# Kernel optimization log

Hardware: AMD Instinct MI355X
Metric: run time of the kernel (lower is better)

The kernel has to match this reference:

```python
import jax, jax.numpy as jnp
import numpy as np

B, T, D, H, P = 2, 2048, 1024, 16, 64  # batch, seq, d_model, heads, head_dim


def setup_inputs() -> dict:
    key = jax.random.key(0)
    ks = jax.random.split(key, 8)
    s = 0.02
    return {
        "Q": jax.random.normal(ks[0], (B, T, D), jnp.float32),
        "K": jax.random.normal(ks[1], (B, T, D), jnp.float32),
        "V": jax.random.normal(ks[2], (B, T, D), jnp.float32),
        "mask": jnp.ones((B, 1, 1, T), jnp.float32),
        "WQ": jax.random.normal(ks[3], (H, D, P), jnp.float32) * s,
        "WK": jax.random.normal(ks[4], (H, D, P), jnp.float32) * s,
        "WV": jax.random.normal(ks[5], (H, D, P), jnp.float32) * s,
        "rel_emb": jax.random.normal(ks[6], (2 * T - 1, P), jnp.float32) * s,
        "dense_W": jax.random.normal(ks[7], (H * P, D), jnp.float32) * s,
        "dense_b": jnp.zeros((D,), jnp.float32),
    }


def reference(Q, K, V, mask, WQ, WK, WV, rel_emb, dense_W, dense_b):
    # multi-head projections: (B,T,D) x (H,D,P) -> (B,H,T,P)
    q = jnp.einsum("btd,hdp->bhtp", Q, WQ)
    k = jnp.einsum("btd,hdp->bhtp", K, WK)
    v = jnp.einsum("btd,hdp->bhtp", V, WV)

    Tq = q.shape[2]
    # Shaw-style additive relative positional encoding from Q:
    # bias[b,h,i,j] = q[b,h,i] . rel_emb[j - i + T - 1]
    a = jnp.einsum("bhtp,rp->bhtr", q, rel_emb)          # (B,H,T,2T-1)
    rel_idx = jnp.arange(Tq)[None, :] - jnp.arange(Tq)[:, None] + (Tq - 1)  # (T,T)
    rpe = jnp.take_along_axis(a, rel_idx[None, None], axis=-1)              # (B,H,T,T)

    scale = 1.0 / jnp.sqrt(jnp.asarray(P, q.dtype))
    energies = (jnp.einsum("bhtp,bhsp->bhts", q, k) + rpe) * scale
    energies = energies + (1.0 - mask) * -1e9
    alphas = jax.nn.softmax(energies, axis=-1)
    ctx = jnp.einsum("bhts,bhsp->bhtp", alphas, v)        # (B,H,T,P)

    ctx = jnp.transpose(ctx, (0, 2, 1, 3)).reshape(ctx.shape[0], Tq, H * P)
    return ctx @ dense_W + dense_b
```

## Files before the change

### kernel.cpp

```cpp
#include <hip/hip_runtime.h>
#include <hip/hip_bf16.h>

typedef __bf16 bf16_t;
typedef __bf16 bf16x2 __attribute__((ext_vector_type(2)));
typedef __bf16 bf16x8 __attribute__((ext_vector_type(8)));
typedef float f32x4 __attribute__((ext_vector_type(4)));

#define QSCALE 0.1803368801111396f
#define MLOG2E 1.4426950408889634f
#define MCONST 12.0f

__device__ __forceinline__ f32x4 mfma16(bf16x8 a, bf16x8 b, f32x4 c) {
  return __builtin_amdgcn_mfma_f32_16x16x32_bf16(a, b, c, 0, 0, 0);
}

#define GLDS16(gsrc, ldst)                                                     \
  __builtin_amdgcn_global_load_lds(                                            \
      (const __attribute__((address_space(1))) void*)(gsrc),                   \
      (__attribute__((address_space(3))) void*)(ldst), 16, 0, 0)

__device__ __forceinline__ unsigned pack2(float a, float b) {
  bf16x2 t = {(bf16_t)a, (bf16_t)b};
  return __builtin_bit_cast(unsigned, t);
}
__device__ __forceinline__ unsigned short bbits(bf16_t v) {
  return __builtin_bit_cast(unsigned short, v);
}

__global__ void conv_kernel(const float* __restrict__ Q,
                            const float* __restrict__ K,
                            const float* __restrict__ V,
                            const float* __restrict__ WQ,
                            const float* __restrict__ WK,
                            const float* __restrict__ WV,
                            const float* __restrict__ dW,
                            bf16_t* __restrict__ qf, bf16_t* __restrict__ kf,
                            bf16_t* __restrict__ vf, bf16_t* __restrict__ wqf,
                            bf16_t* __restrict__ wkf, bf16_t* __restrict__ wvf,
                            bf16_t* __restrict__ dwf) {
  const int y = blockIdx.y;
  const float* s;
  bf16_t* d;
  size_t n;
  switch (y) {
    case 0: s = Q;  d = qf;  n = 4194304; break;
    case 1: s = K;  d = kf;  n = 4194304; break;
    case 2: s = V;  d = vf;  n = 4194304; break;
    case 3: s = WQ; d = wqf; n = 1048576; break;
    case 4: s = WK; d = wkf; n = 1048576; break;
    case 5: s = WV; d = wvf; n = 1048576; break;
    default: s = dW; d = dwf; n = 1048576; break;
  }
  size_t i = ((size_t)blockIdx.x * 256 + threadIdx.x) * 8;
  if (i >= n) return;
  float4 a = *(const float4*)(s + i);
  float4 b = *(const float4*)(s + i + 4);
  uint4 u = {pack2(a.x, a.y), pack2(a.z, a.w), pack2(b.x, b.y),
             pack2(b.z, b.w)};
  *(uint4*)(d + i) = u;
}

__global__ void prep_kernel(const float* __restrict__ rel,
                            const float* __restrict__ mask,
                            bf16_t* __restrict__ relb,
                            float* __restrict__ mbias) {
  int idx = blockIdx.x * 256 + threadIdx.x;
  if (idx < 4096 * 64) {
    int row = idx >> 6;
    int col = idx & 63;
    int sr = row > 4094 ? 4094 : row;
    relb[idx] = (bf16_t)rel[sr * 64 + col];
  } else {
    int j = idx - 4096 * 64;
    if (j < 4096) mbias[j] = (1.0f - mask[j]) * -1e9f * MLOG2E;
  }
}

__global__ __launch_bounds__(256) void proj_gemm_kernel(
    const bf16_t* __restrict__ Qf, const bf16_t* __restrict__ Kf,
    const bf16_t* __restrict__ Vf, const bf16_t* __restrict__ WQf,
    const bf16_t* __restrict__ WKf, const bf16_t* __restrict__ WVf,
    bf16_t* __restrict__ qb, bf16_t* __restrict__ kb,
    bf16_t* __restrict__ vb) {
  const int z = blockIdx.z;
  const bf16_t* A = z == 0 ? Qf : (z == 1 ? Kf : Vf);
  const bf16_t* W = z == 0 ? WQf : (z == 1 ? WKf : WVf);
  bf16_t* out = z == 0 ? qb : (z == 1 ? kb : vb);
  const float scale = z == 0 ? QSCALE : 1.0f;

  __shared__ bf16_t As[128][72];
  __shared__ bf16_t Bs[128][72];
  const int tid = threadIdx.x;
  const int lane = tid & 63;
  const int wid = tid >> 6;
  const int wm = wid >> 1, wn = wid & 1;
  const int row0 = blockIdx.x * 128;
  const int col0 = blockIdx.y * 128;
  const int lr = lane & 15;
  const int lk = (lane >> 4) * 8;

  f32x4 acc[4][4];
#pragma unroll
  for (int m = 0; m < 4; m++)
#pragma unroll
    for (int n = 0; n < 4; n++) acc[m][n] = {0.f, 0.f, 0.f, 0.f};

  for (int kt = 0; kt < 1024; kt += 64) {
#pragma unroll
    for (int i = 0; i < 4; i++) {
      int c = tid + i * 256;
      int row = c >> 3;
      int k8 = (c & 7) * 8;
      *(uint4*)&As[row][k8] =
          *(const uint4*)(A + (size_t)(row0 + row) * 1024 + kt + k8);
    }
#pragma unroll
    for (int i = 0; i < 4; i++) {
      int c = tid + i * 256;
      int col = c & 127;
      int k8 = (c >> 7) * 8;
      int gcol = col0 + col;
      int h = gcol >> 6, p = gcol & 63;
      const bf16_t* src = W + (size_t)h * 65536 + (size_t)(kt + k8) * 64 + p;
      unsigned short b0 = bbits(src[0]), b1 = bbits(src[64]);
      unsigned short b2 = bbits(src[128]), b3 = bbits(src[192]);
      unsigned short b4 = bbits(src[256]), b5 = bbits(src[320]);
      unsigned short b6 = bbits(src[384]), b7 = bbits(src[448]);
      uint4 u = {(unsigned)b0 | ((unsigned)b1 << 16),
                 (unsigned)b2 | ((unsigned)b3 << 16),
                 (unsigned)b4 | ((unsigned)b5 << 16),
                 (unsigned)b6 | ((unsigned)b7 << 16)};
      *(uint4*)&Bs[col][k8] = u;
    }
    __syncthreads();
#pragma unroll
    for (int kk = 0; kk < 2; kk++) {
      bf16x8 af[4], bfr[4];
#pragma unroll
      for (int m = 0; m < 4; m++)
        af[m] = *(const bf16x8*)&As[wm * 64 + m * 16 + lr][kk * 32 + lk];
#pragma unroll
      for (int n = 0; n < 4; n++)
        bfr[n] = *(const bf16x8*)&Bs[wn * 64 + n * 16 + lr][kk * 32 + lk];
#pragma unroll
      for (int m = 0; m < 4; m++)
#pragma unroll
        for (int n = 0; n < 4; n++)
          acc[m][n] = mfma16(af[m], bfr[n], acc[m][n]);
    }
    __syncthreads();
  }
  const int rb = (lane >> 4) * 4;
#pragma unroll
  for (int m = 0; m < 4; m++) {
#pragma unroll
    for (int n = 0; n < 4; n++) {
      int col = col0 + wn * 64 + n * 16 + lr;
      int h = col >> 6, p = col & 63;
      int row_base = row0 + wm * 64 + m * 16 + rb;
      int b = row_base >> 11, t0 = row_base & 2047;
      if (z == 2) {
        uint2 u = {pack2(acc[m][n][0], acc[m][n][1]),
                   pack2(acc[m][n][2], acc[m][n][3])};
        *(uint2*)&out[(((size_t)(b * 16 + h) * 64 + p) * 2048) + t0] = u;
      } else {
#pragma unroll
        for (int r = 0; r < 4; r++) {
          out[(((size_t)(b * 16 + h) * 2048 + t0 + r) * 64) + p] =
              (bf16_t)(acc[m][n][r] * scale);
        }
      }
    }
  }
}

__global__ __launch_bounds__(256) void dense_gemm_kernel(
    const bf16_t* __restrict__ A, const bf16_t* __restrict__ W,
    const float* __restrict__ bias, float* __restrict__ out) {
  __shared__ bf16_t As[128][72];
  __shared__ bf16_t Bs[128][72];
  const int tid = threadIdx.x;
  const int lane = tid & 63;
  const int wid = tid >> 6;
  const int wm = wid >> 1, wn = wid & 1;
  const int row0 = blockIdx.x * 128;
  const int col0 = blockIdx.y * 128;
  const int lr = lane & 15;
  const int lk = (lane >> 4) * 8;

  f32x4 acc[4][4];
#pragma unroll
  for (int m = 0; m < 4; m++)
#pragma unroll
    for (int n = 0; n < 4; n++) acc[m][n] = {0.f, 0.f, 0.f, 0.f};

  for (int kt = 0; kt < 1024; kt += 64) {
#pragma unroll
    for (int i = 0; i < 4; i++) {
      int c = tid + i * 256;
      int row = c >> 3;
      int k8 = (c & 7) * 8;
      *(uint4*)&As[row][k8] =
          *(const uint4*)(A + (size_t)(row0 + row) * 1024 + kt + k8);
    }
#pragma unroll
    for (int i = 0; i < 4; i++) {
      int c = tid + i * 256;
      int col = c & 127;
      int k8 = (c >> 7) * 8;
      const bf16_t* src = W + (size_t)(kt + k8) * 1024 + col0 + col;
      unsigned short b0 = bbits(src[0]), b1 = bbits(src[1024]);
      unsigned short b2 = bbits(src[2048]), b3 = bbits(src[3072]);
      unsigned short b4 = bbits(src[4096]), b5 = bbits(src[5120]);
      unsigned short b6 = bbits(src[6144]), b7 = bbits(src[7168]);
      uint4 u = {(unsigned)b0 | ((unsigned)b1 << 16),
                 (unsigned)b2 | ((unsigned)b3 << 16),
                 (unsigned)b4 | ((unsigned)b5 << 16),
                 (unsigned)b6 | ((unsigned)b7 << 16)};
      *(uint4*)&Bs[col][k8] = u;
    }
    __syncthreads();
#pragma unroll
    for (int kk = 0; kk < 2; kk++) {
      bf16x8 af[4], bfr[4];
#pragma unroll
      for (int m = 0; m < 4; m++)
        af[m] = *(const bf16x8*)&As[wm * 64 + m * 16 + lr][kk * 32 + lk];
#pragma unroll
      for (int n = 0; n < 4; n++)
        bfr[n] = *(const bf16x8*)&Bs[wn * 64 + n * 16 + lr][kk * 32 + lk];
#pragma unroll
      for (int m = 0; m < 4; m++)
#pragma unroll
        for (int n = 0; n < 4; n++)
          acc[m][n] = mfma16(af[m], bfr[n], acc[m][n]);
    }
    __syncthreads();
  }
  const int rb = (lane >> 4) * 4;
#pragma unroll
  for (int m = 0; m < 4; m++) {
#pragma unroll
    for (int n = 0; n < 4; n++) {
      int col = col0 + wn * 64 + n * 16 + lr;
      float bv = bias[col];
#pragma unroll
      for (int r = 0; r < 4; r++) {
        int row = row0 + wm * 64 + m * 16 + rb + r;
        out[(size_t)row * 1024 + col] = acc[m][n][r] + bv;
      }
    }
  }
}

__global__ __launch_bounds__(256, 2) void attn_kernel(
    const bf16_t* __restrict__ qg, const bf16_t* __restrict__ kg,
    const bf16_t* __restrict__ vt, const bf16_t* __restrict__ relb,
    const float* __restrict__ mbias, bf16_t* __restrict__ ctx) {
  __shared__ bf16_t Kb[2][64 * 64];
  __shared__ bf16_t Vb[2][64 * 64];
  __shared__ bf16_t Rr[4][64 * 64];
  __shared__ unsigned SC[4][688];

  const int tid = threadIdx.x;
  const int lane = tid & 63;
  const int w = tid >> 6;

  const int id = blockIdx.x;
  const int id2 = (id & 7) * 64 + (id >> 3);
  const int it = id2 & 15;
  const int bh = id2 >> 4;
  const int h = bh & 15;
  const int b = bh >> 4;
  const int i0 = it * 128;

  const size_t base = ((size_t)bh) * 2048 * 64;
  const int lr = lane & 15;
  const int g = lane >> 4;
  const int lk = g * 8;
  const int srow = lane >> 3;
  const int t16 = lane & 7;
  const int swz = (lr & 7) << 3;

  const bf16_t* kgb = kg + base;
  const bf16_t* vgb = vt + base;
  const bf16_t* rgb = relb + (size_t)(1920 - i0) * 64;

  bf16x8 aq[2][2];
#pragma unroll
  for (int gq = 0; gq < 2; gq++) {
    const bf16_t* src =
        qg + base + (size_t)(i0 + w * 32 + gq * 16 + lr) * 64 + lk;
    aq[gq][0] = *(const bf16x8*)(src);
    aq[gq][1] = *(const bf16x8*)(src + 32);
  }

  float l0 = 0.f, l1 = 0.f;
  f32x4 o0[4], o1[4];
#pragma unroll
  for (int n = 0; n < 4; n++) {
    o0[n] = {0.f, 0.f, 0.f, 0.f};
    o1[n] = {0.f, 0.f, 0.f, 0.f};
  }

  const float* mb_base = mbias + (size_t)b * 2048;
  unsigned* scw = SC[w];
  int sh[4];
#pragma unroll
  for (int r = 0; r < 4; r++) sh[r] = ((r + lr + 1) & 1) << 4;

#pragma unroll
  for (int i = 0; i < 2; i++) {
    int chunk = i * 4 + w;
    int row = chunk * 8 + srow;
    GLDS16(kgb + row * 64 + ((t16 ^ (row & 7)) * 8),
           Kb[0] + chunk * 512 + lane * 8);
  }
#pragma unroll
  for (int i = 0; i < 2; i++) {
    int chunk = i * 4 + w;
    int p = chunk * 8 + srow;
    GLDS16(vgb + (size_t)p * 2048 + ((t16 ^ (p & 7)) * 8),
           Vb[0] + chunk * 512 + lane * 8);
  }
#pragma unroll
  for (int c = 0; c < 3; c++) {
#pragma unroll
    for (int i = 0; i < 2; i++) {
      int chunk = i * 4 + w;
      int row = chunk * 8 + srow;
      GLDS16(rgb + (size_t)(c * 64 + row) * 64 + ((t16 ^ (row & 7)) * 8),
             Rr[c] + chunk * 512 + lane * 8);
    }
  }
  __syncthreads();

  for (int jt = 0; jt < 32; jt++) {
    const int j0 = jt * 64;

    f32x4 mbv[4];
#pragma unroll
    for (int n = 0; n < 4; n++)
      mbv[n] = *(const f32x4*)&mb_base[j0 + n * 16 + g * 4];

    if (jt < 31) {
#pragma unroll
      for (int i = 0; i < 2; i++) {
        int chunk = i * 4 + w;
        int p = chunk * 8 + srow;
        GLDS16(vgb + (j0 + 64) + (size_t)p * 2048 + ((t16 ^ (p & 7)) * 8),
               Vb[(jt + 1) & 1] + chunk * 512 + lane * 8);
      }
      const bf16_t* kn = kgb + (size_t)(j0 + 64) * 64;
      bf16_t* kd = Kb[(jt + 1) & 1];
#pragma unroll
      for (int i = 0; i < 2; i++) {
        int chunk = i * 4 + w;
        int row = chunk * 8 + srow;
        GLDS16(kn + row * 64 + ((t16 ^ (row & 7)) * 8),
               kd + chunk * 512 + lane * 8);
      }
      const bf16_t* rs = rgb + (size_t)(jt + 3) * 64 * 64;
      bf16_t* rd = Rr[(jt + 3) & 3];
#pragma unroll
      for (int i = 0; i < 2; i++) {
        int chunk = i * 4 + w;
        int row = chunk * 8 + srow;
        GLDS16(rs + row * 64 + ((t16 ^ (row & 7)) * 8),
               rd + chunk * 512 + lane * 8);
      }
    }

    f32x4 sacc0[4], sacc1[4], er0[5], er1[5];
#pragma unroll
    for (int n = 0; n < 4; n++) {
      sacc0[n] = {0.f, 0.f, 0.f, 0.f};
      sacc1[n] = {0.f, 0.f, 0.f, 0.f};
    }
#pragma unroll
    for (int n = 0; n < 5; n++) {
      er0[n] = {0.f, 0.f, 0.f, 0.f};
      er1[n] = {0.f, 0.f, 0.f, 0.f};
    }
    const bf16_t* kcur = Kb[jt & 1];
    __builtin_amdgcn_s_setprio(1);
#pragma unroll
    for (int kk = 0; kk < 2; kk++) {
      int cbs = (kk * 32 + lk) ^ swz;
#pragma unroll
      for (int n = 0; n < 4; n++) {
        bf16x8 ak = *(const bf16x8*)&kcur[(n * 16 + lr) * 64 + cbs];
        sacc0[n] = mfma16(ak, aq[0][kk], sacc0[n]);
        sacc1[n] = mfma16(ak, aq[1][kk], sacc1[n]);
      }
#pragma unroll
      for (int fi = 0; fi < 6; fi++) {
        int f = 6 - 2 * w + fi;
        const bf16_t* rc = Rr[(jt + (f >> 2)) & 3];
        bf16x8 ar = *(const bf16x8*)&rc[((f & 3) * 16 + lr) * 64 + cbs];
        if (fi >= 1) er0[fi - 1] = mfma16(ar, aq[0][kk], er0[fi - 1]);
        if (fi <= 4) er1[fi] = mfma16(ar, aq[1][kk], er1[fi]);
      }
    }
    __builtin_amdgcn_s_setprio(0);

    const bf16_t* vcur = Vb[jt & 1];
    bf16x8 av[2][4];

    {
#pragma unroll
      for (int n2 = 0; n2 < 5; n2++) {
        uint2 u = {pack2(er0[n2][0], er0[n2][1]), pack2(er0[n2][2], er0[n2][3])};
        *(uint2*)&scw[lr * 42 + n2 * 8 + g * 2] = u;
      }
      float ps = 0.f;
      float e[4][4];
#pragma unroll
      for (int n = 0; n < 4; n++) {
#pragma unroll
        for (int r = 0; r < 4; r++) {
          int key = n * 16 + g * 4 + r;
          int idx = key - lr + 15;
          unsigned d = scw[lr * 42 + (idx >> 1)];
          float bias = __builtin_bit_cast(float, (d >> sh[r]) << 16);
          float s = sacc0[n][r] + bias + mbv[n][r];
          e[n][r] = exp2f(s - MCONST);
          ps += e[n][r];
        }
      }
      l0 += ps;
#pragma unroll
      for (int n = 0; n < 4; n++) {
        uint2 u = {pack2(e[n][0], e[n][1]), pack2(e[n][2], e[n][3])};
        *(uint2*)&scw[lr * 36 + n * 8 + g * 2] = u;
      }
      bf16x8 bp0[2];
      bp0[0] = __builtin_bit_cast(bf16x8, *(const uint4*)&scw[lr * 36 + g * 4]);
      bp0[1] =
          __builtin_bit_cast(bf16x8, *(const uint4*)&scw[lr * 36 + 16 + g * 4]);
#pragma unroll
      for (int kk = 0; kk < 2; kk++) {
        int cbs = (kk * 32 + lk) ^ swz;
#pragma unroll
        for (int n = 0; n < 4; n++)
          av[kk][n] = *(const bf16x8*)&vcur[(n * 16 + lr) * 64 + cbs];
      }
      __builtin_amdgcn_s_setprio(1);
#pragma unroll
      for (int kk = 0; kk < 2; kk++)
#pragma unroll
        for (int n = 0; n < 4; n++) o0[n] = mfma16(av[kk][n], bp0[kk], o0[n]);
      __builtin_amdgcn_s_setprio(0);
    }

    {
#pragma unroll
      for (int n2 = 0; n2 < 5; n2++) {
        uint2 u = {pack2(er1[n2][0], er1[n2][1]), pack2(er1[n2][2], er1[n2][3])};
        *(uint2*)&scw[lr * 42 + n2 * 8 + g * 2] = u;
      }
      float ps = 0.f;
      float e[4][4];
#pragma unroll
      for (int n = 0; n < 4; n++) {
#pragma unroll
        for (int r = 0; r < 4; r++) {
          int key = n * 16 + g * 4 + r;
          int idx = key - lr + 15;
          unsigned d = scw[lr * 42 + (idx >> 1)];
          float bias = __builtin_bit_cast(float, (d >> sh[r]) << 16);
          float s = sacc1[n][r] + bias + mbv[n][r];
          e[n][r] = exp2f(s - MCONST);
          ps += e[n][r];
        }
      }
      l1 += ps;
#pragma unroll
      for (int n = 0; n < 4; n++) {
        uint2 u = {pack2(e[n][0], e[n][1]), pack2(e[n][2], e[n][3])};
        *(uint2*)&scw[lr * 36 + n * 8 + g * 2] = u;
      }
      bf16x8 bp1[2];
      bp1[0] = __builtin_bit_cast(bf16x8, *(const uint4*)&scw[lr * 36 + g * 4]);
      bp1[1] =
          __builtin_bit_cast(bf16x8, *(const uint4*)&scw[lr * 36 + 16 + g * 4]);
      __builtin_amdgcn_s_setprio(1);
#pragma unroll
      for (int kk = 0; kk < 2; kk++)
#pragma unroll
        for (int n = 0; n < 4; n++) o1[n] = mfma16(av[kk][n], bp1[kk], o1[n]);
      __builtin_amdgcn_s_setprio(0);
    }

    __syncthreads();
  }

  l0 += __shfl_xor(l0, 16, 64);
  l0 += __shfl_xor(l0, 32, 64);
  l1 += __shfl_xor(l1, 16, 64);
  l1 += __shfl_xor(l1, 32, 64);

#pragma unroll
  for (int gq = 0; gq < 2; gq++) {
    f32x4* o = gq ? o1 : o0;
    float inv = 1.0f / (gq ? l1 : l0);
    size_t bt = (size_t)b * 2048 + i0 + w * 32 + gq * 16 + lr;
#pragma unroll
    for (int n = 0; n < 4; n++) {
      uint2 u = {pack2(o[n][0] * inv, o[n][1] * inv),
                 pack2(o[n][2] * inv, o[n][3] * inv)};
      *(uint2*)&ctx[bt * 1024 + h * 64 + n * 16 + g * 4] = u;
    }
  }
}

extern "C" void kernel_launch(void* const* d_in, const int* in_sizes, int n_in,
                              void* d_out, int out_size, void* d_ws,
                              size_t ws_size, hipStream_t stream) {
  (void)in_sizes; (void)n_in; (void)out_size; (void)ws_size;
  const float* Q    = (const float*)d_in[0];
  const float* K    = (const float*)d_in[1];
  const float* V    = (const float*)d_in[2];
  const float* mask = (const float*)d_in[3];
  const float* WQ   = (const float*)d_in[4];
  const float* WK   = (const float*)d_in[5];
  const float* WV   = (const float*)d_in[6];
  const float* rel  = (const float*)d_in[7];
  const float* dW   = (const float*)d_in[8];
  const float* db   = (const float*)d_in[9];
  float* out = (float*)d_out;

  const size_t N4M = (size_t)4096 * 1024;
  const size_t N1M = (size_t)1024 * 1024;
  bf16_t* qf   = (bf16_t*)d_ws;
  bf16_t* kf   = qf + N4M;
  bf16_t* vf   = kf + N4M;
  bf16_t* wqf  = vf + N4M;
  bf16_t* wkf  = wqf + N1M;
  bf16_t* wvf  = wkf + N1M;
  bf16_t* dwf  = wvf + N1M;
  bf16_t* qb   = dwf + N1M;
  bf16_t* kb   = qb + N4M;
  bf16_t* vb   = kb + N4M;
  bf16_t* ctxb = vb + N4M;
  bf16_t* relb = ctxb + N4M;
  float*  mbias = (float*)(relb + 4096 * 64);

  dim3 blk(256);
  conv_kernel<<<dim3(2048, 7), blk, 0, stream>>>(Q, K, V, WQ, WK, WV, dW, qf,
                                                 kf, vf, wqf, wkf, wvf, dwf);
  prep_kernel<<<dim3((4096 * 64 + 4096) / 256), blk, 0, stream>>>(rel, mask,
                                                                  relb, mbias);
  proj_gemm_kernel<<<dim3(32, 8, 3), blk, 0, stream>>>(qf, kf, vf, wqf, wkf,
                                                       wvf, qb, kb, vb);
  attn_kernel<<<dim3(512), blk, 0, stream>>>(qb, kb, vb, relb, mbias, ctxb);
  dense_gemm_kernel<<<dim3(32, 8), blk, 0, stream>>>(ctxb, dwf, db, out);
}
```

Baseline: 194.2 us.

## Pre-transpose weights to K-major bf16 and load GEMM tiles via direct-to-LDS swizzle

A new transpose kernel converts the projection and dense weights to bf16 in a K-contiguous (N x K) layout, replacing the plain conversion of those weights. Both GEMM kernels then fill their A and B tiles with global_load_lds 16-byte transfers into an unpadded LDS layout with an XOR swizzle. This removes the eight strided 2-byte gathers per thread for the B operand and the register round trip through VGPRs. The cost is one extra launch and a transpose pass that uses LDS.

```diff
diff --git a/kernel.cpp b/kernel.cpp
--- a/kernel.cpp
+++ b/kernel.cpp
@@ -23,41 +23,66 @@
   bf16x2 t = {(bf16_t)a, (bf16_t)b};
   return __builtin_bit_cast(unsigned, t);
 }
-__device__ __forceinline__ unsigned short bbits(bf16_t v) {
-  return __builtin_bit_cast(unsigned short, v);
-}
 
 __global__ void conv_kernel(const float* __restrict__ Q,
                             const float* __restrict__ K,
                             const float* __restrict__ V,
-                            const float* __restrict__ WQ,
-                            const float* __restrict__ WK,
-                            const float* __restrict__ WV,
-                            const float* __restrict__ dW,
                             bf16_t* __restrict__ qf, bf16_t* __restrict__ kf,
-                            bf16_t* __restrict__ vf, bf16_t* __restrict__ wqf,
-                            bf16_t* __restrict__ wkf, bf16_t* __restrict__ wvf,
-                            bf16_t* __restrict__ dwf) {
+                            bf16_t* __restrict__ vf) {
   const int y = blockIdx.y;
-  const float* s;
-  bf16_t* d;
-  size_t n;
-  switch (y) {
-    case 0: s = Q;  d = qf;  n = 4194304; break;
-    case 1: s = K;  d = kf;  n = 4194304; break;
-    case 2: s = V;  d = vf;  n = 4194304; break;
-    case 3: s = WQ; d = wqf; n = 1048576; break;
-    case 4: s = WK; d = wkf; n = 1048576; break;
-    case 5: s = WV; d = wvf; n = 1048576; break;
-    default: s = dW; d = dwf; n = 1048576; break;
-  }
+  const float* s = y == 0 ? Q : (y == 1 ? K : V);
+  bf16_t* d = y == 0 ? qf : (y == 1 ? kf : vf);
   size_t i = ((size_t)blockIdx.x * 256 + threadIdx.x) * 8;
-  if (i >= n) return;
   float4 a = *(const float4*)(s + i);
   float4 b = *(const float4*)(s + i + 4);
   uint4 u = {pack2(a.x, a.y), pack2(a.z, a.w), pack2(b.x, b.y),
              pack2(b.z, b.w)};
   *(uint4*)(d + i) = u;
+}
+
+__global__ void transpose_w_kernel(const float* __restrict__ WQ,
+                                   const float* __restrict__ WK,
+                                   const float* __restrict__ WV,
+                                   const float* __restrict__ dW,
+                                   bf16_t* __restrict__ wqt,
+                                   bf16_t* __restrict__ wkt,
+                                   bf16_t* __restrict__ wvt,
+                                   bf16_t* __restrict__ dwt) {
+  __shared__ float tl[64][65];
+  const int mat = blockIdx.y;
+  const float* s = mat == 0 ? WQ : (mat == 1 ? WK : (mat == 2 ? WV : dW));
+  bf16_t* d = mat == 0 ? wqt : (mat == 1 ? wkt : (mat == 2 ? wvt : dwt));
+  const int tile = blockIdx.x;
+  int row0, col0;
+  size_t sstride;
+  const float* sp;
+  if (mat < 3) {
+    int h = tile >> 4;
+    row0 = (tile & 15) * 64;
+    col0 = h * 64;
+    sstride = 64;
+    sp = s + (size_t)h * 65536 + (size_t)row0 * 64;
+  } else {
+    int nt = tile >> 4;
+    row0 = (tile & 15) * 64;
+    col0 = nt * 64;
+    sstride = 1024;
+    sp = s + (size_t)row0 * 1024 + (size_t)nt * 64;
+  }
+  const int t = threadIdx.x;
+#pragma unroll
+  for (int i = 0; i < 16; i++) {
+    int lin = t + i * 256;
+    int r = lin >> 6, c = lin & 63;
+    tl[r][c] = sp[(size_t)r * sstride + c];
+  }
+  __syncthreads();
+#pragma unroll
+  for (int i = 0; i < 16; i++) {
+    int lin = t + i * 256;
+    int p = lin >> 6, k = lin & 63;
+    d[(size_t)(col0 + p) * 1024 + row0 + k] = (bf16_t)tl[k][p];
+  }
 }
 
 __global__ void prep_kernel(const float* __restrict__ rel,
@@ -78,18 +103,18 @@
 
 __global__ __launch_bounds__(256) void proj_gemm_kernel(
     const bf16_t* __restrict__ Qf, const bf16_t* __restrict__ Kf,
-    const bf16_t* __restrict__ Vf, const bf16_t* __restrict__ WQf,
-    const bf16_t* __restrict__ WKf, const bf16_t* __restrict__ WVf,
+    const bf16_t* __restrict__ Vf, const bf16_t* __restrict__ WQt,
+    const bf16_t* __restrict__ WKt, const bf16_t* __restrict__ WVt,
     bf16_t* __restrict__ qb, bf16_t* __restrict__ kb,
     bf16_t* __restrict__ vb) {
   const int z = blockIdx.z;
   const bf16_t* A = z == 0 ? Qf : (z == 1 ? Kf : Vf);
-  const bf16_t* W = z == 0 ? WQf : (z == 1 ? WKf : WVf);
+  const bf16_t* Wt = z == 0 ? WQt : (z == 1 ? WKt : WVt);
   bf16_t* out = z == 0 ? qb : (z == 1 ? kb : vb);
   const float scale = z == 0 ? QSCALE : 1.0f;
 
-  __shared__ bf16_t As[128][72];
-  __shared__ bf16_t Bs[128][72];
+  __shared__ bf16_t As[128 * 64];
+  __shared__ bf16_t Bs[128 * 64];
   const int tid = threadIdx.x;
   const int lane = tid & 63;
   const int wid = tid >> 6;
@@ -98,6 +123,9 @@
   const int col0 = blockIdx.y * 128;
   const int lr = lane & 15;
   const int lk = (lane >> 4) * 8;
+  const int srow = lane >> 3;
+  const int t16 = lane & 7;
+  const int swz = (lr & 7) << 3;
 
   f32x4 acc[4][4];
 #pragma unroll
@@ -108,40 +136,25 @@
   for (int kt = 0; kt < 1024; kt += 64) {
 #pragma unroll
     for (int i = 0; i < 4; i++) {
-      int c = tid + i * 256;
-      int row = c >> 3;
-      int k8 = (c & 7) * 8;
-      *(uint4*)&As[row][k8] =
-          *(const uint4*)(A + (size_t)(row0 + row) * 1024 + kt + k8);
-    }
-#pragma unroll
-    for (int i = 0; i < 4; i++) {
-      int c = tid + i * 256;
-      int col = c & 127;
-      int k8 = (c >> 7) * 8;
-      int gcol = col0 + col;
-      int h = gcol >> 6, p = gcol & 63;
-      const bf16_t* src = W + (size_t)h * 65536 + (size_t)(kt + k8) * 64 + p;
-      unsigned short b0 = bbits(src[0]), b1 = bbits(src[64]);
-      unsigned short b2 = bbits(src[128]), b3 = bbits(src[192]);
-      unsigned short b4 = bbits(src[256]), b5 = bbits(src[320]);
-      unsigned short b6 = bbits(src[384]), b7 = bbits(src[448]);
-      uint4 u = {(unsigned)b0 | ((unsigned)b1 << 16),
-                 (unsigned)b2 | ((unsigned)b3 << 16),
-                 (unsigned)b4 | ((unsigned)b5 << 16),
-                 (unsigned)b6 | ((unsigned)b7 << 16)};
-      *(uint4*)&Bs[col][k8] = u;
+      int chunk = i * 4 + wid;
+      int row = chunk * 8 + srow;
+      int so = (t16 ^ (row & 7)) * 8;
+      GLDS16(A + (size_t)(row0 + row) * 1024 + kt + so,
+             As + chunk * 512 + lane * 8);
+      GLDS16(Wt + (size_t)(col0 + row) * 1024 + kt + so,
+             Bs + chunk * 512 + lane * 8);
     }
     __syncthreads();
 #pragma unroll
     for (int kk = 0; kk < 2; kk++) {
+      int cbs = (kk * 32 + lk) ^ swz;
       bf16x8 af[4], bfr[4];
 #pragma unroll
       for (int m = 0; m < 4; m++)
-        af[m] = *(const bf16x8*)&As[wm * 64 + m * 16 + lr][kk * 32 + lk];
+        af[m] = *(const bf16x8*)&As[(wm * 64 + m * 16 + lr) * 64 + cbs];
 #pragma unroll
       for (int n = 0; n < 4; n++)
-        bfr[n] = *(const bf16x8*)&Bs[wn * 64 + n * 16 + lr][kk * 32 + lk];
+        bfr[n] = *(const bf16x8*)&Bs[(wn * 64 + n * 16 + lr) * 64 + cbs];
 #pragma unroll
       for (int m = 0; m < 4; m++)
 #pragma unroll
@@ -175,10 +188,10 @@
 }
 
 __global__ __launch_bounds__(256) void dense_gemm_kernel(
-    const bf16_t* __restrict__ A, const bf16_t* __restrict__ W,
+    const bf16_t* __restrict__ A, const bf16_t* __restrict__ Wt,
     const float* __restrict__ bias, float* __restrict__ out) {
-  __shared__ bf16_t As[128][72];
-  __shared__ bf16_t Bs[128][72];
+  __shared__ bf16_t As[128 * 64];
+  __shared__ bf16_t Bs[128 * 64];
   const int tid = threadIdx.x;
   const int lane = tid & 63;
   const int wid = tid >> 6;
@@ -187,6 +200,9 @@
   const int col0 = blockIdx.y * 128;
   const int lr = lane & 15;
   const int lk = (lane >> 4) * 8;
+  const int srow = lane >> 3;
+  const int t16 = lane & 7;
+  const int swz = (lr & 7) << 3;
 
   f32x4 acc[4][4];
 #pragma unroll
@@ -197,38 +213,25 @@
   for (int kt = 0; kt < 1024; kt += 64) {
 #pragma unroll
     for (int i = 0; i < 4; i++) {
-      int c = tid + i * 256;
-      int row = c >> 3;
-      int k8 = (c & 7) * 8;
-      *(uint4*)&As[row][k8] =
-          *(const uint4*)(A + (size_t)(row0 + row) * 1024 + kt + k8);
-    }
-#pragma unroll
-    for (int i = 0; i < 4; i++) {
-      int c = tid + i * 256;
-      int col = c & 127;
-      int k8 = (c >> 7) * 8;
-      const bf16_t* src = W + (size_t)(kt + k8) * 1024 + col0 + col;
-      unsigned short b0 = bbits(src[0]), b1 = bbits(src[1024]);
-      unsigned short b2 = bbits(src[2048]), b3 = bbits(src[3072]);
-      unsigned short b4 = bbits(src[4096]), b5 = bbits(src[5120]);
-      unsigned short b6 = bbits(src[6144]), b7 = bbits(src[7168]);
-      uint4 u = {(unsigned)b0 | ((unsigned)b1 << 16),
-                 (unsigned)b2 | ((unsigned)b3 << 16),
-                 (unsigned)b4 | ((unsigned)b5 << 16),
-                 (unsigned)b6 | ((unsigned)b7 << 16)};
-      *(uint4*)&Bs[col][k8] = u;
+      int chunk = i * 4 + wid;
+      int row = chunk * 8 + srow;
+      int so = (t16 ^ (row & 7)) * 8;
+      GLDS16(A + (size_t)(row0 + row) * 1024 + kt + so,
+             As + chunk * 512 + lane * 8);
+      GLDS16(Wt + (size_t)(col0 + row) * 1024 + kt + so,
+             Bs + chunk * 512 + lane * 8);
     }
     __syncthreads();
 #pragma unroll
     for (int kk = 0; kk < 2; kk++) {
+      int cbs = (kk * 32 + lk) ^ swz;
       bf16x8 af[4], bfr[4];
 #pragma unroll
       for (int m = 0; m < 4; m++)
-        af[m] = *(const bf16x8*)&As[wm * 64 + m * 16 + lr][kk * 32 + lk];
+        af[m] = *(const bf16x8*)&As[(wm * 64 + m * 16 + lr) * 64 + cbs];
 #pragma unroll
       for (int n = 0; n < 4; n++)
-        bfr[n] = *(const bf16x8*)&Bs[wn * 64 + n * 16 + lr][kk * 32 + lk];
+        bfr[n] = *(const bf16x8*)&Bs[(wn * 64 + n * 16 + lr) * 64 + cbs];
 #pragma unroll
       for (int m = 0; m < 4; m++)
 #pragma unroll
@@ -535,11 +538,11 @@
   bf16_t* qf   = (bf16_t*)d_ws;
   bf16_t* kf   = qf + N4M;
   bf16_t* vf   = kf + N4M;
-  bf16_t* wqf  = vf + N4M;
-  bf16_t* wkf  = wqf + N1M;
-  bf16_t* wvf  = wkf + N1M;
-  bf16_t* dwf  = wvf + N1M;
-  bf16_t* qb   = dwf + N1M;
+  bf16_t* wqt  = vf + N4M;
+  bf16_t* wkt  = wqt + N1M;
+  bf16_t* wvt  = wkt + N1M;
+  bf16_t* dwt  = wvt + N1M;
+  bf16_t* qb   = dwt + N1M;
   bf16_t* kb   = qb + N4M;
   bf16_t* vb   = kb + N4M;
   bf16_t* ctxb = vb + N4M;
@@ -547,12 +550,13 @@
   float*  mbias = (float*)(relb + 4096 * 64);
 
   dim3 blk(256);
-  conv_kernel<<<dim3(2048, 7), blk, 0, stream>>>(Q, K, V, WQ, WK, WV, dW, qf,
-                                                 kf, vf, wqf, wkf, wvf, dwf);
+  conv_kernel<<<dim3(2048, 3), blk, 0, stream>>>(Q, K, V, qf, kf, vf);
+  transpose_w_kernel<<<dim3(256, 4), blk, 0, stream>>>(WQ, WK, WV, dW, wqt,
+                                                       wkt, wvt, dwt);
   prep_kernel<<<dim3((4096 * 64 + 4096) / 256), blk, 0, stream>>>(rel, mask,
                                                                   relb, mbias);
-  proj_gemm_kernel<<<dim3(32, 8, 3), blk, 0, stream>>>(qf, kf, vf, wqf, wkf,
-                                                       wvf, qb, kb, vb);
+  proj_gemm_kernel<<<dim3(32, 8, 3), blk, 0, stream>>>(qf, kf, vf, wqt, wkt,
+                                                       wvt, qb, kb, vb);
   attn_kernel<<<dim3(512), blk, 0, stream>>>(qb, kb, vb, relb, mbias, ctxb);
-  dense_gemm_kernel<<<dim3(32, 8), blk, 0, stream>>>(ctxb, dwf, db, out);
-}
+  dense_gemm_kernel<<<dim3(32, 8), blk, 0, stream>>>(ctxb, dwt, db, out);
+}
```

New measurement: 186.7 us. 3.9% less time.
